# Optimization experiments

Measured on AMD Instinct MI355X. Metric: run time of the kernel, lower is better.

The kernel has to match this reference:

```python
import jax, jax.numpy as jnp
import numpy as np
from jax.scipy.linalg import solve_triangular

EPS = 1e-5
CHUNK = 64

def _rms(x, w, eps=EPS):
    return x * jax.lax.rsqrt(jnp.mean(x * x, axis=-1, keepdims=True) + eps) * w

def _l2norm(x, eps=1e-6):
    return x * jax.lax.rsqrt(jnp.sum(x * x, axis=-1, keepdims=True) + eps)

def _causal_conv(x, w):
    # x: [B,T,C], w: [C,K] depthwise causal short conv
    K = w.shape[1]
    T = x.shape[1]
    xp = jnp.pad(x, ((0, 0), (K - 1, 0), (0, 0)))
    return sum(xp[:, j:j + T, :] * w[:, j] for j in range(K))

def _chunk_gated_delta_rule(q, k, v, g, beta, chunk=CHUNK):
    # q,k: [B,H,T,Dk] (l2-normalized, q pre-scaled); v: [B,H,T,Dv]; g,beta: [B,H,T]
    Bb, H, T, Dk = k.shape
    Dv = v.shape[-1]
    N = T // chunk
    qc, kc, vc = (a.reshape(Bb, H, N, chunk, -1) for a in (q, k, v))
    gc = g.reshape(Bb, H, N, chunk)
    bc = beta.reshape(Bb, H, N, chunk)
    gcs = jnp.cumsum(gc, axis=-1)  # within-chunk cumulative log-decay
    tri = jnp.tril(jnp.ones((chunk, chunk), bool))
    tri_s = jnp.tril(jnp.ones((chunk, chunk), bool), -1)
    diff = gcs[..., :, None] - gcs[..., None, :]
    decay = jnp.where(tri, jnp.exp(jnp.where(tri, diff, 0.0)), 0.0)  # [B,H,N,C,C]
    k_beta = kc * bc[..., None]
    v_beta = vc * bc[..., None]
    A = jnp.einsum('bhnck,bhndk->bhncd', k_beta, kc) * decay
    A = jnp.where(tri_s, A, 0.0)
    eye = jnp.eye(chunk, dtype=q.dtype)
    Tmat = solve_triangular(eye + A, jnp.broadcast_to(eye, A.shape), lower=True)  # (I+A)^-1
    u = Tmat @ v_beta                               # [B,H,N,C,Dv]
    w = Tmat @ (k_beta * jnp.exp(gcs)[..., None])   # [B,H,N,C,Dk]

    def step(S, inp):
        q_i, k_i, u_i, w_i, g_i, dm_i = inp
        attn = jnp.where(tri, jnp.einsum('bhck,bhdk->bhcd', q_i, k_i) * dm_i, 0.0)
        v_new = u_i - w_i @ S
        o_i = (q_i * jnp.exp(g_i)[..., None]) @ S + attn @ v_new
        g_last = g_i[..., -1]
        k_dec = k_i * jnp.exp(g_last[..., None] - g_i)[..., None]
        S = S * jnp.exp(g_last)[..., None, None] + jnp.einsum('bhck,bhcv->bhkv', k_dec, v_new)
        return S, o_i

    xs = tuple(jnp.moveaxis(a, 2, 0) for a in (qc, kc, u, w, gcs, decay))
    S0 = jnp.zeros((Bb, H, Dk, Dv), q.dtype)
    _, outs = jax.lax.scan(step, S0, xs)  # [N,B,H,C,Dv]
    return jnp.moveaxis(outs, 0, 2).reshape(Bb, H, T, Dv)

def _layer_forward(x, mask, ln1_w, qkvz_w, ba_w, conv_w, A_log, dt_bias,
                   o_norm_w, out_w, ln2_w, gate_w, up_w, down_w):
    B, T, D = x.shape
    H = A_log.shape[0]
    kd = qkvz_w.shape[0] // 4  # key_dim == value_dim here (k_heads==v_heads, Dk==Dv)
    vd = kd
    Dk = kd // H
    Dv = vd // H
    silu = jax.nn.silu
    h = _rms(x, ln1_w)
    qkvz = h @ qkvz_w.T
    q, k, v, z = jnp.split(qkvz, [kd, 2 * kd, 2 * kd + vd], axis=-1)
    b, a = jnp.split(h @ ba_w.T, 2, axis=-1)  # [B,T,H] each
    mixed = jnp.concatenate([q, k, v], axis=-1) * mask[..., None]
    mixed = silu(_causal_conv(mixed, conv_w))
    q, k, v = jnp.split(mixed, [kd, 2 * kd], axis=-1)
    q = _l2norm(q.reshape(B, T, H, Dk))
    k = _l2norm(k.reshape(B, T, H, Dk))
    v = v.reshape(B, T, H, Dv)
    beta = jax.nn.sigmoid(b) * mask[..., None]
    g = -jnp.exp(A_log) * jax.nn.softplus(a + dt_bias) * mask[..., None]
    scale = Dk ** -0.5
    bhtd = lambda t: jnp.transpose(t, (0, 2, 1, 3))
    o = _chunk_gated_delta_rule(bhtd(q) * scale, bhtd(k), bhtd(v),
                                jnp.transpose(g, (0, 2, 1)), jnp.transpose(beta, (0, 2, 1)))
    o = jnp.transpose(o, (0, 2, 1, 3))  # [B,T,H,Dv]
    o = _rms(o, o_norm_w) * silu(z.reshape(B, T, H, Dv))  # gated RMSNorm
    x = x + o.reshape(B, T, vd) @ out_w.T
    h2 = _rms(x, ln2_w)
    mlp_out = (silu(h2 @ gate_w.T) * (h2 @ up_w.T)) @ down_w.T
    return x + mlp_out

def setup_inputs():
    key = jax.random.key(0)
    ks = jax.random.split(key, 12)
    B, T, D, H, Dk, Dv, M, K = 1, 4096, 2048, 16, 128, 128, 8192, 4
    kd, vd = H * Dk, H * Dv
    nrm = lambda i, shp, sc=0.02: jax.random.normal(ks[i], shp, jnp.float32) * sc
    return {
        'x': nrm(0, (B, T, D), 1.0),
        'mask': jnp.ones((B, T), jnp.float32),
        'ln1_w': jnp.ones((D,), jnp.float32),
        'qkvz_w': nrm(1, (2 * kd + 2 * vd, D)),
        'ba_w': nrm(2, (2 * H, D)),
        'conv_w': nrm(3, (2 * kd + vd, K), 0.3),
        'A_log': jnp.log(jax.random.uniform(ks[4], (H,), jnp.float32, 1.0, 16.0)),
        'dt_bias': nrm(5, (H,), 0.5),
        'o_norm_w': jnp.ones((Dv,), jnp.float32),
        'out_w': nrm(6, (D, vd)),
        'ln2_w': jnp.ones((D,), jnp.float32),
        'gate_w': nrm(7, (M, D)),
        'up_w': nrm(8, (M, D)),
        'down_w': nrm(9, (D, M)),
    }

def reference(x, mask, ln1_w, qkvz_w, ba_w, conv_w, A_log, dt_bias,
              o_norm_w, out_w, ln2_w, gate_w, up_w, down_w):
    return _layer_forward(x, mask, ln1_w, qkvz_w, ba_w, conv_w, A_log, dt_bias,
                          o_norm_w, out_w, ln2_w, gate_w, up_w, down_w)
```

## Files before the change

kernel.cpp:

```cpp
#include <hip/hip_runtime.h>
#include <math.h>

#define T_LEN 4096
#define DMODEL 2048
#define NH 16
#define CQKV 6144
#define CQKVZ 8192
#define SCALE 0.08838834764831845f

using bf16x8 = __attribute__((ext_vector_type(8))) short;
using f32x4  = __attribute__((ext_vector_type(4))) float;

__device__ __forceinline__ float siluf(float x) { return x / (1.0f + __expf(-x)); }

__device__ __forceinline__ unsigned short f2bf(float f) {
  unsigned int u = __float_as_uint(f);
  u = (u + 0x7FFFu + ((u >> 16) & 1u)) >> 16;
  return (unsigned short)u;
}
__device__ __forceinline__ float bf2f(unsigned short u) {
  return __uint_as_float(((unsigned int)u) << 16);
}
__device__ __forceinline__ ushort4 pack4(float a, float b, float c, float d) {
  ushort4 r; r.x = f2bf(a); r.y = f2bf(b); r.z = f2bf(c); r.w = f2bf(d); return r;
}

__device__ __forceinline__ void gl_lds16(const unsigned short* g, unsigned short* l) {
  __builtin_amdgcn_global_load_lds(
      (const __attribute__((address_space(1))) void*)g,
      (__attribute__((address_space(3))) void*)l, 16, 0, 0);
}

template<int MODE>
__global__ __launch_bounds__(256) void rmsnorm_kernel(const float* __restrict__ x,
                                                      const float* __restrict__ w,
                                                      float* __restrict__ outf,
                                                      unsigned short* __restrict__ outb) {
  const int t = blockIdx.x;
  const int tid = threadIdx.x;
  const float4* xr = (const float4*)(x + (size_t)t * DMODEL);
  float4 v0 = xr[tid];
  float4 v1 = xr[tid + 256];
  float s = v0.x*v0.x + v0.y*v0.y + v0.z*v0.z + v0.w*v0.w
          + v1.x*v1.x + v1.y*v1.y + v1.z*v1.z + v1.w*v1.w;
#pragma unroll
  for (int off = 32; off > 0; off >>= 1) s += __shfl_down(s, off);
  __shared__ float red[4];
  if ((tid & 63) == 0) red[tid >> 6] = s;
  __syncthreads();
  const float tot = red[0] + red[1] + red[2] + red[3];
  const float r = rsqrtf(tot * (1.0f / DMODEL) + 1e-5f);
  const float4* wr = (const float4*)w;
  const float4 w0 = wr[tid], w1 = wr[tid + 256];
  float4 o0, o1;
  o0.x = v0.x*r*w0.x; o0.y = v0.y*r*w0.y; o0.z = v0.z*r*w0.z; o0.w = v0.w*r*w0.w;
  o1.x = v1.x*r*w1.x; o1.y = v1.y*r*w1.y; o1.z = v1.z*r*w1.z; o1.w = v1.w*r*w1.w;
  if (MODE == 1) {
    float4* orow = (float4*)(outf + (size_t)t * DMODEL);
    orow[tid] = o0;
    orow[tid + 256] = o1;
  }
  ushort4* brow = (ushort4*)(outb + (size_t)t * DMODEL);
  brow[tid] = pack4(o0.x, o0.y, o0.z, o0.w);
  brow[tid + 256] = pack4(o1.x, o1.y, o1.z, o1.w);
}

__global__ __launch_bounds__(256) void f2b_kernel(const float* __restrict__ in,
                                                  unsigned short* __restrict__ out) {
  const size_t i = (size_t)blockIdx.x * 256 + threadIdx.x;
  const float4 a = ((const float4*)in)[2 * i];
  const float4 b = ((const float4*)in)[2 * i + 1];
  ((ushort4*)out)[2 * i] = pack4(a.x, a.y, a.z, a.w);
  ((ushort4*)out)[2 * i + 1] = pack4(b.x, b.y, b.z, b.w);
}

template<int EPI, int BM>
__global__ __launch_bounds__(512, 1) void gemm256_kernel(const unsigned short* __restrict__ A,
                                                         const unsigned short* __restrict__ B,
                                                         float* __restrict__ Cf,
                                                         unsigned short* __restrict__ Cb,
                                                         int M, int N, int K) {
  constexpr int BN = 256;
  constexpr int MI = BM / 32;
  constexpr int AW = BM / 128;
  __shared__ __align__(16) unsigned short lds[3][(BM + BN) * 32];
  const int nbm = M / BM, nbn = N / BN, nwg = nbm * nbn;
  const int nt = K >> 5;
  int bmi, bni;
  {
    const int bid = blockIdx.x;
    const int cpx = nwg >> 3;
    int sc = 1;
    while (sc * sc < cpx) sc <<= 1;
    if (sc * sc > cpx) sc >>= 1;
    const int scn = (sc > 0) ? (cpx / sc) : 0;
    if ((nwg & 7) == 0 && sc > 0 && sc * scn == cpx && (nbm % sc) == 0 && (nbn % scn) == 0) {
      const int chunk = bid & 7, widx = bid >> 3;
      const int regc = nbn / scn;
      bmi = (chunk / regc) * sc + widx / scn;
      bni = (chunk % regc) * scn + widx % scn;
    } else {
      bmi = bid / nbn; bni = bid % nbn;
    }
  }
  const int bm = bmi * BM, bn = bni * BN;
  const int tid = threadIdx.x;
  const int wv = tid >> 6, ln = tid & 63;
  const int fr = ln & 15, qq = ln >> 4;
  const int wm = wv >> 2, wn = wv & 3;
  const int ra0 = wm * (BM / 2), rb0 = wn * 64;
  const int lrow = ln >> 2;
  const int lslot = ln & 3;

  f32x4 acc[MI][4];
  const f32x4 zero = {0.f, 0.f, 0.f, 0.f};
#pragma unroll
  for (int mi = 0; mi < MI; mi++)
#pragma unroll
    for (int ni = 0; ni < 4; ni++) acc[mi][ni] = zero;

  auto stageA = [&](int buf, int t) {
    const int k0 = t << 5;
#pragma unroll
    for (int q = 0; q < AW; q++) {
      const int lr = q * 128 + wv * 16 + lrow;
      const int sl = lslot ^ ((lr >> 1) & 3);
      gl_lds16(A + (size_t)(bm + lr) * K + k0 + sl * 8,
               &lds[buf][(q * 128 + wv * 16) * 32]);
    }
  };
  auto stageB = [&](int buf, int t) {
    const int k0 = t << 5;
#pragma unroll
    for (int q = 0; q < 2; q++) {
      const int lr = q * 128 + wv * 16 + lrow;
      const int sl = lslot ^ ((lr >> 1) & 3);
      gl_lds16(B + (size_t)(bn + lr) * K + k0 + sl * 8,
               &lds[buf][BM * 32 + (q * 128 + wv * 16) * 32]);
    }
  };

  stageA(0, 0); stageB(0, 0);
  stageA(1, 1); stageB(1, 1);
  if constexpr (AW == 2) asm volatile("s_waitcnt vmcnt(4)" ::: "memory");
  else                   asm volatile("s_waitcnt vmcnt(3)" ::: "memory");
  __builtin_amdgcn_s_barrier();
  asm volatile("" ::: "memory");

  for (int t = 0; t < nt; t++) {
    const int cb = t % 3;
    const int b2 = (t + 2) % 3;
    const unsigned short* lA = &lds[cb][0];
    const unsigned short* lB = &lds[cb][BM * 32];
    bf16x8 bfr[4];
#pragma unroll
    for (int ni = 0; ni < 4; ni++) {
      const int r = rb0 + ni * 16 + fr;
      bfr[ni] = *(const bf16x8*)&lB[r * 32 + ((qq ^ ((r >> 1) & 3)) << 3)];
    }
    bf16x8 afr[MI];
#pragma unroll
    for (int mi = 0; mi < MI; mi++) {
      const int r = ra0 + mi * 16 + fr;
      afr[mi] = *(const bf16x8*)&lA[r * 32 + ((qq ^ ((r >> 1) & 3)) << 3)];
    }
    if (t + 2 < nt) { stageA(b2, t + 2); stageB(b2, t + 2); }
    __builtin_amdgcn_s_setprio(1);
#pragma unroll
    for (int mi = 0; mi < MI; mi++)
#pragma unroll
      for (int ni = 0; ni < 4; ni++)
        acc[mi][ni] = __builtin_amdgcn_mfma_f32_16x16x32_bf16(afr[mi], bfr[ni], acc[mi][ni], 0, 0, 0);
    __builtin_amdgcn_s_setprio(0);
    if (t + 1 < nt) {
      asm volatile("s_waitcnt lgkmcnt(0)" ::: "memory");
      if (t + 2 < nt) {
        if constexpr (AW == 2) asm volatile("s_waitcnt vmcnt(4)" ::: "memory");
        else                   asm volatile("s_waitcnt vmcnt(3)" ::: "memory");
      } else {
        asm volatile("s_waitcnt vmcnt(0)" ::: "memory");
      }
      __builtin_amdgcn_s_barrier();
      asm volatile("" ::: "memory");
    }
  }

  const int cm4 = qq * 4;
#pragma unroll
  for (int mi = 0; mi < MI; mi++) {
#pragma unroll
    for (int ni = 0; ni < 4; ni++) {
#pragma unroll
      for (int r = 0; r < 4; r++) {
        const int grow = bm + ra0 + mi * 16 + cm4 + r;
        const int gcol = bn + rb0 + ni * 16 + fr;
        const size_t off = (size_t)grow * N + gcol;
        const float v = acc[mi][ni][r];
        if (EPI == 0) {
          Cb[off] = f2bf(v);
        } else if (EPI == 1) {
          Cf[off] += v;
        } else {
          Cb[off] = f2bf(siluf(bf2f(Cb[off])) * v);
        }
      }
    }
  }
}

__global__ __launch_bounds__(256) void ba_gemm_kernel(const float* __restrict__ h_in,
                                                      const float* __restrict__ ba_w,
                                                      float* __restrict__ ba_out) {
  __shared__ __align__(16) float hl[2048];
  __shared__ float red[32][9];
  const int t = blockIdx.x;
  const int tid = threadIdx.x;
  const float4* hr = (const float4*)(h_in + (size_t)t * DMODEL);
  ((float4*)hl)[tid] = hr[tid];
  ((float4*)hl)[tid + 256] = hr[tid + 256];
  __syncthreads();
  const int c = tid & 31;
  const int p = tid >> 5;
  const float* wrow = ba_w + (size_t)c * DMODEL + p * 256;
  const float* hrow = hl + p * 256;
  float s = 0.f;
#pragma unroll 8
  for (int k = 0; k < 256; k++) s += hrow[k] * wrow[k];
  red[c][p] = s;
  __syncthreads();
  if (tid < 32) {
    float tot = 0.f;
#pragma unroll
    for (int q = 0; q < 8; q++) tot += red[tid][q];
    ba_out[(size_t)t * 32 + tid] = tot;
  }
}

__global__ __launch_bounds__(256) void zcopy_kernel(const unsigned short* __restrict__ qkvz,
                                                    unsigned short* __restrict__ z) {
  const int idx = blockIdx.x * 256 + threadIdx.x;
  const int t = idx >> 8;
  const int c8 = (idx & 255) * 8;
  *(uint4*)(z + (size_t)t * 2048 + c8) =
      *(const uint4*)(qkvz + (size_t)t * CQKVZ + CQKV + c8);
}

__global__ __launch_bounds__(256) void conv_silu_kernel(const unsigned short* __restrict__ qkvz,
                                                        const float* __restrict__ conv_w,
                                                        const float* __restrict__ mask,
                                                        float* __restrict__ mixed) {
  const int idx = blockIdx.x * 256 + threadIdx.x;
  const int c4 = (idx % 1536) * 4;
  const int t = idx / 1536;
  const float4 w0 = *(const float4*)(conv_w + (size_t)c4 * 4);
  const float4 w1 = *(const float4*)(conv_w + (size_t)c4 * 4 + 4);
  const float4 w2 = *(const float4*)(conv_w + (size_t)c4 * 4 + 8);
  const float4 w3 = *(const float4*)(conv_w + (size_t)c4 * 4 + 12);
  const float wj0[4] = {w0.x, w0.y, w0.z, w0.w};
  const float wj1[4] = {w1.x, w1.y, w1.z, w1.w};
  const float wj2[4] = {w2.x, w2.y, w2.z, w2.w};
  const float wj3[4] = {w3.x, w3.y, w3.z, w3.w};
  float4 acc = make_float4(0.f, 0.f, 0.f, 0.f);
#pragma unroll
  for (int j = 0; j < 4; j++) {
    const int tt = t - 3 + j;
    if (tt < 0) continue;
    const float m = mask[tt];
    const ushort4 xb = *(const ushort4*)(qkvz + (size_t)tt * CQKVZ + c4);
    acc.x += bf2f(xb.x) * m * wj0[j];
    acc.y += bf2f(xb.y) * m * wj1[j];
    acc.z += bf2f(xb.z) * m * wj2[j];
    acc.w += bf2f(xb.w) * m * wj3[j];
  }
  acc.x = siluf(acc.x); acc.y = siluf(acc.y); acc.z = siluf(acc.z); acc.w = siluf(acc.w);
  *(float4*)(mixed + (size_t)t * CQKV + c4) = acc;
}

__global__ __launch_bounds__(256) void l2norm_kernel(float* __restrict__ mixed) {
  const int r = blockIdx.x * 4 + (threadIdx.x >> 6);
  const int lane = threadIdx.x & 63;
  const int t = r >> 5;
  const int hh = r & 31;
  float* p = mixed + (size_t)t * CQKV + hh * 128 + lane * 2;
  float2 v = *(float2*)p;
  float s = v.x * v.x + v.y * v.y;
#pragma unroll
  for (int off = 32; off > 0; off >>= 1) s += __shfl_down(s, off);
  s = __shfl(s, 0);
  const float rn = rsqrtf(s + 1e-6f);
  v.x *= rn; v.y *= rn;
  *(float2*)p = v;
}

__global__ __launch_bounds__(256) void beta_g_kernel(const float* __restrict__ ba,
                                                     const float* __restrict__ A_log,
                                                     const float* __restrict__ dt_bias,
                                                     const float* __restrict__ mask,
                                                     float* __restrict__ beta,
                                                     float* __restrict__ g) {
  const int idx = blockIdx.x * 256 + threadIdx.x;
  const int t = idx >> 4;
  const int h = idx & 15;
  const float b = ba[(size_t)t * 32 + h];
  const float a = ba[(size_t)t * 32 + 16 + h];
  const float m = mask[t];
  beta[idx] = m / (1.0f + expf(-b));
  const float xx = a + dt_bias[h];
  const float sp = (xx > 20.0f) ? xx : log1pf(expf(xx));
  g[idx] = -expf(A_log[h]) * sp * m;
}

__global__ __launch_bounds__(256) void gcs_kernel(const float* __restrict__ g,
                                                  float* __restrict__ gcsbuf,
                                                  float* __restrict__ edkbuf,
                                                  float* __restrict__ egqbuf,
                                                  float* __restrict__ adecbuf) {
  const int idx = blockIdx.x * 256 + threadIdx.x;
  if (idx >= 1024) return;
  const int h = idx >> 6;
  const int n = idx & 63;
  const int t0 = n * 64;
  float s = 0.f;
  for (int i = 0; i < 64; i++) {
    s += g[(size_t)(t0 + i) * NH + h];
    gcsbuf[(size_t)idx * 64 + i] = s;
  }
  const float glast = s;
  adecbuf[idx] = __expf(glast);
  for (int i = 0; i < 64; i++) {
    const float gi = gcsbuf[(size_t)idx * 64 + i];
    edkbuf[(size_t)idx * 64 + i] = __expf(glast - gi);
    egqbuf[(size_t)idx * 64 + i] = __expf(gi) * SCALE;
  }
}

__global__ __launch_bounds__(256) void pre_attn_kernel(const float* __restrict__ mixed,
                                                       const float* __restrict__ gcsbuf,
                                                       const float* __restrict__ betabuf,
                                                       float* __restrict__ abuf,
                                                       float* __restrict__ attnbuf) {
  __shared__ __align__(16) float kl[64][132];
  __shared__ float gcs_s[64];
  __shared__ float betal[64];
  const int blk = blockIdx.x;
  const int h = blk >> 6;
  const int n = blk & 63;
  const int t0 = n * 64;
  const int tid = threadIdx.x;
  if (tid < 64) {
    gcs_s[tid] = gcsbuf[(size_t)blk * 64 + tid];
    betal[tid] = betabuf[(size_t)(t0 + tid) * NH + h];
  }
#pragma unroll
  for (int rep = 0; rep < 8; rep++) {
    const int lin = rep * 256 + tid;
    const int i = lin >> 5;
    const int d = (lin & 31) * 4;
    const float4 kv = *(const float4*)(mixed + (size_t)(t0 + i) * CQKV + 2048 + h * 128 + d);
    *(float4*)&kl[i][d] = kv;
  }
  __syncthreads();
  const int cj = tid & 15;
  const int ri = tid >> 4;
  const int i0 = ri * 4, j0 = cj * 4;
  float accA[4][4], accQ[4][4];
#pragma unroll
  for (int a = 0; a < 4; a++)
#pragma unroll
    for (int b = 0; b < 4; b++) { accA[a][b] = 0.f; accQ[a][b] = 0.f; }
  const float* qbase = mixed + (size_t)t0 * CQKV + h * 128;
#pragma unroll 4
  for (int d = 0; d < 128; d++) {
    const float kj0 = kl[j0][d], kj1 = kl[j0 + 1][d], kj2 = kl[j0 + 2][d], kj3 = kl[j0 + 3][d];
#pragma unroll
    for (int a = 0; a < 4; a++) {
      const float ka = kl[i0 + a][d];
      const float qa = qbase[(size_t)(i0 + a) * CQKV + d];
      accA[a][0] += ka * kj0; accA[a][1] += ka * kj1; accA[a][2] += ka * kj2; accA[a][3] += ka * kj3;
      accQ[a][0] += qa * kj0; accQ[a][1] += qa * kj1; accQ[a][2] += qa * kj2; accQ[a][3] += qa * kj3;
    }
  }
#pragma unroll
  for (int a = 0; a < 4; a++) {
    const int i = i0 + a;
    const float gi = gcs_s[i];
    const float bi = betal[i];
    float4 Av, Qv;
    float dec;
    dec = __expf(fminf(gi - gcs_s[j0 + 0], 0.f));
    Av.x = (i > j0 + 0) ? accA[a][0] * bi * dec : 0.f;
    Qv.x = (i >= j0 + 0) ? accQ[a][0] * dec * SCALE : 0.f;
    dec = __expf(fminf(gi - gcs_s[j0 + 1], 0.f));
    Av.y = (i > j0 + 1) ? accA[a][1] * bi * dec : 0.f;
    Qv.y = (i >= j0 + 1) ? accQ[a][1] * dec * SCALE : 0.f;
    dec = __expf(fminf(gi - gcs_s[j0 + 2], 0.f));
    Av.z = (i > j0 + 2) ? accA[a][2] * bi * dec : 0.f;
    Qv.z = (i >= j0 + 2) ? accQ[a][2] * dec * SCALE : 0.f;
    dec = __expf(fminf(gi - gcs_s[j0 + 3], 0.f));
    Av.w = (i > j0 + 3) ? accA[a][3] * bi * dec : 0.f;
    Qv.w = (i >= j0 + 3) ? accQ[a][3] * dec * SCALE : 0.f;
    *(float4*)(abuf + (size_t)blk * 4096 + i * 64 + j0) = Av;
    *(float4*)(attnbuf + (size_t)blk * 4096 + i * 64 + j0) = Qv;
  }
}

__global__ __launch_bounds__(256) void pre_solve_kernel(const float* __restrict__ abuf,
                                                        const float* __restrict__ betabuf,
                                                        float* __restrict__ tbuf) {
  __shared__ float Al[64][65];
  __shared__ float Tl[64][65];
  const int blk = blockIdx.x;
  const int h = blk >> 6;
  const int n = blk & 63;
  const int t0 = n * 64;
  const int tid = threadIdx.x;
#pragma unroll
  for (int rep = 0; rep < 4; rep++) {
    const int lin = rep * 256 + tid;
    const int i = lin >> 4;
    const int j = (lin & 15) * 4;
    const float4 av = *(const float4*)(abuf + (size_t)blk * 4096 + i * 64 + j);
    Al[i][j] = av.x; Al[i][j + 1] = av.y; Al[i][j + 2] = av.z; Al[i][j + 3] = av.w;
  }
  __syncthreads();
  if (tid < 64) {
    const int j = tid;
    const float bj = betabuf[(size_t)(t0 + j) * NH + h];
    for (int i = 0; i < 64; i++) {
      float s = (i == j) ? 1.0f : 0.0f;
      for (int l = j; l < i; l++) s -= Al[i][l] * Tl[l][j];
      Tl[i][j] = s;
    }
    for (int i = j; i < 64; i++) Tl[i][j] *= bj;
  }
  __syncthreads();
#pragma unroll
  for (int rep = 0; rep < 4; rep++) {
    const int lin = rep * 256 + tid;
    const int i = lin >> 4;
    const int j = (lin & 15) * 4;
    float4 tv;
    tv.x = Tl[i][j]; tv.y = Tl[i][j + 1]; tv.z = Tl[i][j + 2]; tv.w = Tl[i][j + 3];
    *(float4*)(tbuf + (size_t)blk * 4096 + i * 64 + j) = tv;
  }
}

__global__ __launch_bounds__(256) void pre_uw_kernel(const float* __restrict__ mixed,
                                                     const float* __restrict__ tbuf,
                                                     const float* __restrict__ gcsbuf,
                                                     float* __restrict__ ubuf,
                                                     unsigned short* __restrict__ wbf) {
  __shared__ __align__(16) float Tl[64][68];
  __shared__ __align__(16) float xl[64][132];
  __shared__ float egcs[64];
  const int blk = blockIdx.x;
  const int h = blk >> 6;
  const int n = blk & 63;
  const int t0 = n * 64;
  const int tid = threadIdx.x;
  if (tid < 64) egcs[tid] = __expf(gcsbuf[(size_t)blk * 64 + tid]);
#pragma unroll
  for (int rep = 0; rep < 4; rep++) {
    const int lin = rep * 256 + tid;
    const int i = lin >> 4;
    const int j = (lin & 15) * 4;
    const float4 tv = *(const float4*)(tbuf + (size_t)blk * 4096 + i * 64 + j);
    *(float4*)&Tl[i][j] = tv;
  }
#pragma unroll
  for (int rep = 0; rep < 8; rep++) {
    const int lin = rep * 256 + tid;
    const int i = lin >> 5;
    const int d = (lin & 31) * 4;
    const float4 vv = *(const float4*)(mixed + (size_t)(t0 + i) * CQKV + 4096 + h * 128 + d);
    *(float4*)&xl[i][d] = vv;
  }
  __syncthreads();
  const int cgu = tid & 15;
  const int riu = tid >> 4;
  const int i0 = riu * 4;
  const int d0 = cgu * 8;
  float acc[4][8];
#pragma unroll
  for (int a = 0; a < 4; a++)
#pragma unroll
    for (int b = 0; b < 8; b++) acc[a][b] = 0.f;
#pragma unroll 2
  for (int j = 0; j < 64; j++) {
    const float tv[4] = {Tl[i0][j], Tl[i0 + 1][j], Tl[i0 + 2][j], Tl[i0 + 3][j]};
    const float4 x0 = *(const float4*)&xl[j][d0];
    const float4 x1 = *(const float4*)&xl[j][d0 + 4];
    const float xv[8] = {x0.x, x0.y, x0.z, x0.w, x1.x, x1.y, x1.z, x1.w};
#pragma unroll
    for (int a = 0; a < 4; a++)
#pragma unroll
      for (int b = 0; b < 8; b++) acc[a][b] += tv[a] * xv[b];
  }
#pragma unroll
  for (int a = 0; a < 4; a++) {
    float* up = ubuf + (size_t)(t0 + i0 + a) * 2048 + h * 128 + d0;
    *(float4*)up = make_float4(acc[a][0], acc[a][1], acc[a][2], acc[a][3]);
    *(float4*)(up + 4) = make_float4(acc[a][4], acc[a][5], acc[a][6], acc[a][7]);
  }
  __syncthreads();
#pragma unroll
  for (int rep = 0; rep < 8; rep++) {
    const int lin = rep * 256 + tid;
    const int i = lin >> 5;
    const int d = (lin & 31) * 4;
    float4 kv = *(const float4*)(mixed + (size_t)(t0 + i) * CQKV + 2048 + h * 128 + d);
    const float e = egcs[i];
    kv.x *= e; kv.y *= e; kv.z *= e; kv.w *= e;
    *(float4*)&xl[i][d] = kv;
  }
  __syncthreads();
#pragma unroll
  for (int a = 0; a < 4; a++)
#pragma unroll
    for (int b = 0; b < 8; b++) acc[a][b] = 0.f;
#pragma unroll 2
  for (int j = 0; j < 64; j++) {
    const float tv[4] = {Tl[i0][j], Tl[i0 + 1][j], Tl[i0 + 2][j], Tl[i0 + 3][j]};
    const float4 x0 = *(const float4*)&xl[j][d0];
    const float4 x1 = *(const float4*)&xl[j][d0 + 4];
    const float xv[8] = {x0.x, x0.y, x0.z, x0.w, x1.x, x1.y, x1.z, x1.w};
#pragma unroll
    for (int a = 0; a < 4; a++)
#pragma unroll
      for (int b = 0; b < 8; b++) acc[a][b] += tv[a] * xv[b];
  }
#pragma unroll
  for (int a = 0; a < 4; a++) {
    unsigned short* wp = wbf + (size_t)(t0 + i0 + a) * 2048 + h * 128 + d0;
    *(ushort4*)wp = pack4(acc[a][0], acc[a][1], acc[a][2], acc[a][3]);
    *(ushort4*)(wp + 4) = pack4(acc[a][4], acc[a][5], acc[a][6], acc[a][7]);
  }
}

__global__ __launch_bounds__(256) void ktrans_kernel(const float* __restrict__ mixed,
                                                     const float* __restrict__ edkbuf,
                                                     const float* __restrict__ egqbuf,
                                                     unsigned short* __restrict__ kdT,
                                                     unsigned short* __restrict__ qe) {
  __shared__ __align__(16) float kl[64][132];
  __shared__ float edk_s[64];
  __shared__ float egq_s[64];
  const int blk = blockIdx.x;
  const int h = blk >> 6;
  const int n = blk & 63;
  const int t0 = n * 64;
  const int tid = threadIdx.x;
  if (tid < 64) {
    edk_s[tid] = edkbuf[(size_t)blk * 64 + tid];
    egq_s[tid] = egqbuf[(size_t)blk * 64 + tid];
  }
#pragma unroll
  for (int q = 0; q < 8; q++) {
    const int idx = tid + q * 256;
    const int l = idx >> 5, c4 = (idx & 31) * 4;
    *(float4*)&kl[l][c4] = *(const float4*)(mixed + (size_t)(t0 + l) * CQKV + 2048 + h * 128 + c4);
  }
  __syncthreads();
#pragma unroll
  for (int q = 0; q < 4; q++) {
    const int idx = tid + q * 256;
    const int d = idx >> 3, l8 = (idx & 7) * 8;
    float v[8];
#pragma unroll
    for (int j = 0; j < 8; j++) v[j] = kl[l8 + j][d] * edk_s[l8 + j];
    unsigned short* p = kdT + (size_t)blk * 8192 + d * 64 + l8;
    *(ushort4*)p = pack4(v[0], v[1], v[2], v[3]);
    *(ushort4*)(p + 4) = pack4(v[4], v[5], v[6], v[7]);
  }
#pragma unroll
  for (int q = 0; q < 8; q++) {
    const int idx = tid + q * 256;
    const int i = idx >> 5, c4 = (idx & 31) * 4;
    const float4 v = *(const float4*)(mixed + (size_t)(t0 + i) * CQKV + h * 128 + c4);
    const float e = egq_s[i];
    *(ushort4*)(qe + (size_t)(t0 + i) * 2048 + h * 128 + c4) =
        pack4(v.x * e, v.y * e, v.z * e, v.w * e);
  }
}

__global__ __launch_bounds__(512) void scan_kernel(const unsigned short* __restrict__ wbf,
                                                   const unsigned short* __restrict__ kdT,
                                                   const float* __restrict__ ubuf,
                                                   const float* __restrict__ adecbuf,
                                                   unsigned short* __restrict__ STb,
                                                   unsigned short* __restrict__ vtb,
                                                   const float* __restrict__ gw,
                                                   const float* __restrict__ uw,
                                                   const float* __restrict__ dw,
                                                   const float* __restrict__ ow,
                                                   const float* __restrict__ xin,
                                                   unsigned short* __restrict__ Wg,
                                                   unsigned short* __restrict__ Wu,
                                                   unsigned short* __restrict__ Wd,
                                                   unsigned short* __restrict__ Wo,
                                                   float* __restrict__ outc) {
  __shared__ __align__(16) unsigned short w_lds[64 * 128];
  __shared__ __align__(16) unsigned short kT_lds[128 * 64];
  __shared__ __align__(16) unsigned short st_lds[128 * 128];
  __shared__ __align__(16) unsigned short vt_lds[128 * 64];
  __shared__ __align__(16) float u_lds[64 * 132];
  if (blockIdx.x >= 16) {
    const int xb = blockIdx.x - 16;
    const int tid = threadIdx.x;
    if (xb < 13312) {
      const float* src;
      unsigned short* dst;
      size_t u;
      if (xb < 4096)       { src = gw; dst = Wg; u = (size_t)xb * 512 + tid; }
      else if (xb < 8192)  { src = uw; dst = Wu; u = (size_t)(xb - 4096) * 512 + tid; }
      else if (xb < 12288) { src = dw; dst = Wd; u = (size_t)(xb - 8192) * 512 + tid; }
      else                 { src = ow; dst = Wo; u = (size_t)(xb - 12288) * 512 + tid; }
      const float4 a = ((const float4*)src)[2 * u];
      const float4 b = ((const float4*)src)[2 * u + 1];
      ((ushort4*)dst)[2 * u] = pack4(a.x, a.y, a.z, a.w);
      ((ushort4*)dst)[2 * u + 1] = pack4(b.x, b.y, b.z, b.w);
    } else {
      const size_t i = (size_t)(xb - 13312) * 512 + tid;
      ((float4*)outc)[i] = ((const float4*)xin)[i];
    }
    return;
  }
  const int h = blockIdx.x;
  const int tid = threadIdx.x;
  const int ln = tid & 63;
  const int wv = tid >> 6;
  const int fr = ln & 15;
  const int g = ln >> 4;
  const int lt = wv & 3;
  const int ch = wv >> 2;
  const f32x4 zero = {0.f, 0.f, 0.f, 0.f};

  uint4 wreg[2], kreg[2];
  float4 ureg[4];
#pragma unroll
  for (int q = 0; q < 2; q++) {
    const int idx = tid + q * 512;
    const int row = idx >> 4, c8 = (idx & 15) * 8;
    wreg[q] = *(const uint4*)(wbf + (size_t)row * 2048 + h * 128 + c8);
    const int d = idx >> 3, l8 = (idx & 7) * 8;
    kreg[q] = *(const uint4*)(kdT + (size_t)(h * 64) * 8192 + d * 64 + l8);
  }
#pragma unroll
  for (int q = 0; q < 4; q++) {
    const int idx = tid + q * 512;
    const int row = idx >> 5, c4 = (idx & 31) * 4;
    ureg[q] = *(const float4*)(ubuf + (size_t)row * 2048 + h * 128 + c4);
  }

  f32x4 acc2[8];
#pragma unroll
  for (int ct = 0; ct < 8; ct++) acc2[ct] = zero;

  for (int n = 0; n < 64; n++) {
    const int blk = h * 64 + n;
#pragma unroll
    for (int q = 0; q < 2; q++) {
      const int idx = tid + q * 512;
      const int row = idx >> 4, c8 = (idx & 15) * 8;
      *(uint4*)&w_lds[row * 128 + (((c8 >> 3) ^ (row & 7)) << 3)] = wreg[q];
    }
#pragma unroll
    for (int q = 0; q < 4; q++) {
      const int idx = tid + q * 512;
      const int row = idx >> 5, c4 = (idx & 31) * 4;
      *(float4*)&u_lds[row * 132 + c4] = ureg[q];
    }
    {
      const int db = wv * 16 + g * 4;
#pragma unroll
      for (int ct = 0; ct < 8; ct++) {
        const int c = ct * 16 + fr;
        *(ushort4*)&st_lds[c * 128 + (((db >> 3) ^ (c & 7)) << 3) + (db & 7)] =
            pack4(acc2[ct][0], acc2[ct][1], acc2[ct][2], acc2[ct][3]);
      }
    }
    asm volatile("s_waitcnt lgkmcnt(0)" ::: "memory");
    __builtin_amdgcn_sched_barrier(0);
    asm volatile("s_barrier" ::: "memory");
    __builtin_amdgcn_sched_barrier(0);
#pragma unroll
    for (int q = 0; q < 2; q++) {
      const int idx = tid + q * 512;
      const int d = idx >> 3, l8 = (idx & 7) * 8;
      *(uint4*)&kT_lds[d * 64 + (((l8 >> 3) ^ (d & 7)) << 3)] = kreg[q];
    }
    if (n < 63) {
      const int t0n = (n + 1) * 64;
#pragma unroll
      for (int q = 0; q < 2; q++) {
        const int idx = tid + q * 512;
        const int row = idx >> 4, c8 = (idx & 15) * 8;
        wreg[q] = *(const uint4*)(wbf + (size_t)(t0n + row) * 2048 + h * 128 + c8);
        const int d = idx >> 3, l8 = (idx & 7) * 8;
        kreg[q] = *(const uint4*)(kdT + (size_t)(blk + 1) * 8192 + d * 64 + l8);
      }
#pragma unroll
      for (int q = 0; q < 4; q++) {
        const int idx = tid + q * 512;
        const int row = idx >> 5, c4 = (idx & 31) * 4;
        ureg[q] = *(const float4*)(ubuf + (size_t)(t0n + row) * 2048 + h * 128 + c4);
      }
    }
#pragma unroll
    for (int q = 0; q < 4; q++) {
      const int idx = tid + q * 512;
      const int c = idx >> 4, dg = idx & 15;
      *(uint4*)(STb + (size_t)blk * 16384 + c * 128 + dg * 8) =
          *(const uint4*)&st_lds[c * 128 + ((dg ^ (c & 7)) << 3)];
    }
    f32x4 acc1[4];
#pragma unroll
    for (int ct = 0; ct < 4; ct++) acc1[ct] = zero;
#pragma unroll
    for (int ks = 0; ks < 4; ks++) {
      const int kb = ks * 4 + g;
      const int ar = lt * 16 + fr;
      const bf16x8 a = *(const bf16x8*)&w_lds[ar * 128 + ((kb ^ (ar & 7)) << 3)];
#pragma unroll
      for (int ct = 0; ct < 4; ct++) {
        const int c = (ch * 4 + ct) * 16 + fr;
        const bf16x8 b = *(const bf16x8*)&st_lds[c * 128 + ((kb ^ (c & 7)) << 3)];
        acc1[ct] = __builtin_amdgcn_mfma_f32_16x16x32_bf16(a, b, acc1[ct], 0, 0, 0);
      }
    }
    {
      const int lb = lt * 16 + g * 4;
#pragma unroll
      for (int ct = 0; ct < 4; ct++) {
        const int c = (ch * 4 + ct) * 16 + fr;
        const float v0 = u_lds[(lb + 0) * 132 + c] - acc1[ct][0];
        const float v1 = u_lds[(lb + 1) * 132 + c] - acc1[ct][1];
        const float v2 = u_lds[(lb + 2) * 132 + c] - acc1[ct][2];
        const float v3 = u_lds[(lb + 3) * 132 + c] - acc1[ct][3];
        *(ushort4*)&vt_lds[c * 64 + (((lb >> 3) ^ (c & 7)) << 3) + (lb & 7)] =
            pack4(v0, v1, v2, v3);
      }
    }
    const float adec = adecbuf[blk];
    asm volatile("s_waitcnt lgkmcnt(0)" ::: "memory");
    __builtin_amdgcn_sched_barrier(0);
    asm volatile("s_barrier" ::: "memory");
    __builtin_amdgcn_sched_barrier(0);
#pragma unroll
    for (int q = 0; q < 2; q++) {
      const int idx = tid + q * 512;
      const int c = idx >> 3, lg = idx & 7;
      *(uint4*)(vtb + (size_t)blk * 8192 + c * 64 + lg * 8) =
          *(const uint4*)&vt_lds[c * 64 + ((lg ^ (c & 7)) << 3)];
    }
#pragma unroll
    for (int ct = 0; ct < 8; ct++) {
      acc2[ct][0] *= adec; acc2[ct][1] *= adec; acc2[ct][2] *= adec; acc2[ct][3] *= adec;
    }
#pragma unroll
    for (int ks = 0; ks < 2; ks++) {
      const int kb = ks * 4 + g;
      const int ar = wv * 16 + fr;
      const bf16x8 a = *(const bf16x8*)&kT_lds[ar * 64 + ((kb ^ (ar & 7)) << 3)];
#pragma unroll
      for (int ct = 0; ct < 8; ct++) {
        const int c = ct * 16 + fr;
        const bf16x8 b = *(const bf16x8*)&vt_lds[c * 64 + ((kb ^ (c & 7)) << 3)];
        acc2[ct] = __builtin_amdgcn_mfma_f32_16x16x32_bf16(a, b, acc2[ct], 0, 0, 0);
      }
    }
  }
}

__global__ __launch_bounds__(256) void ocomp_kernel(const unsigned short* __restrict__ qe,
                                                    const unsigned short* __restrict__ STbuf,
                                                    const unsigned short* __restrict__ vtbuf,
                                                    const float* __restrict__ attnbuf,
                                                    const unsigned short* __restrict__ zb,
                                                    const float* __restrict__ onw,
                                                    unsigned short* __restrict__ ob) {
  __shared__ __align__(16) unsigned short STl[128 * 128];
  __shared__ __align__(16) unsigned short vtl[128 * 64];
  __shared__ __align__(16) unsigned short ql[64 * 128];
  __shared__ __align__(16) unsigned short al[64 * 64];
  const int blk = blockIdx.x;
  const int h = blk >> 6;
  const int n = blk & 63;
  const int t0 = n * 64;
  const int tid = threadIdx.x;
#pragma unroll
  for (int q = 0; q < 8; q++) {
    const int idx = tid + q * 256;
    const int c = idx >> 4, dg = idx & 15;
    *(uint4*)&STl[c * 128 + ((dg ^ (c & 7)) << 3)] =
        *(const uint4*)(STbuf + (size_t)blk * 16384 + c * 128 + dg * 8);
  }
#pragma unroll
  for (int q = 0; q < 4; q++) {
    const int idx = tid + q * 256;
    const int c = idx >> 3, lg = idx & 7;
    *(uint4*)&vtl[c * 64 + ((lg ^ (c & 7)) << 3)] =
        *(const uint4*)(vtbuf + (size_t)blk * 8192 + c * 64 + lg * 8);
  }
#pragma unroll
  for (int q = 0; q < 4; q++) {
    const int idx = tid + q * 256;
    const int i = idx >> 4, dg = idx & 15;
    *(uint4*)&ql[i * 128 + ((dg ^ (i & 7)) << 3)] =
        *(const uint4*)(qe + (size_t)(t0 + i) * 2048 + h * 128 + dg * 8);
  }
#pragma unroll
  for (int q = 0; q < 4; q++) {
    const int idx = tid + q * 256;
    const int i = idx >> 4, l4 = (idx & 15) * 4;
    const float4 v = *(const float4*)(attnbuf + (size_t)blk * 4096 + i * 64 + l4);
    *(ushort4*)&al[i * 64 + (((l4 >> 3) ^ (i & 7)) << 3) + (l4 & 7)] =
        pack4(v.x, v.y, v.z, v.w);
  }
  __syncthreads();
  const int ln = tid & 63;
  const int wv = tid >> 6;
  const int fr = ln & 15;
  const int g = ln >> 4;
  const int i0 = wv * 16;
  f32x4 acc[8];
  const f32x4 zero = {0.f, 0.f, 0.f, 0.f};
#pragma unroll
  for (int nt = 0; nt < 8; nt++) acc[nt] = zero;
#pragma unroll
  for (int ks = 0; ks < 4; ks++) {
    const int kb = ks * 4 + g;
    const int ar = i0 + fr;
    const bf16x8 a = *(const bf16x8*)&ql[ar * 128 + ((kb ^ (ar & 7)) << 3)];
#pragma unroll
    for (int nt = 0; nt < 8; nt++) {
      const int c = nt * 16 + fr;
      const bf16x8 b = *(const bf16x8*)&STl[c * 128 + ((kb ^ (c & 7)) << 3)];
      acc[nt] = __builtin_amdgcn_mfma_f32_16x16x32_bf16(a, b, acc[nt], 0, 0, 0);
    }
  }
#pragma unroll
  for (int ks = 0; ks < 2; ks++) {
    const int kb = ks * 4 + g;
    const int ar = i0 + fr;
    const bf16x8 a = *(const bf16x8*)&al[ar * 64 + ((kb ^ (ar & 7)) << 3)];
#pragma unroll
    for (int nt = 0; nt < 8; nt++) {
      const int c = nt * 16 + fr;
      const bf16x8 b = *(const bf16x8*)&vtl[c * 64 + ((kb ^ (c & 7)) << 3)];
      acc[nt] = __builtin_amdgcn_mfma_f32_16x16x32_bf16(a, b, acc[nt], 0, 0, 0);
    }
  }
  float s0 = 0.f, s1 = 0.f, s2 = 0.f, s3 = 0.f;
#pragma unroll
  for (int nt = 0; nt < 8; nt++) {
    s0 += acc[nt][0] * acc[nt][0];
    s1 += acc[nt][1] * acc[nt][1];
    s2 += acc[nt][2] * acc[nt][2];
    s3 += acc[nt][3] * acc[nt][3];
  }
#pragma unroll
  for (int m = 1; m < 16; m <<= 1) {
    s0 += __shfl_xor(s0, m);
    s1 += __shfl_xor(s1, m);
    s2 += __shfl_xor(s2, m);
    s3 += __shfl_xor(s3, m);
  }
  float rn[4];
  rn[0] = rsqrtf(s0 * (1.0f / 128.0f) + 1e-5f);
  rn[1] = rsqrtf(s1 * (1.0f / 128.0f) + 1e-5f);
  rn[2] = rsqrtf(s2 * (1.0f / 128.0f) + 1e-5f);
  rn[3] = rsqrtf(s3 * (1.0f / 128.0f) + 1e-5f);
#pragma unroll
  for (int nt = 0; nt < 8; nt++) {
    const int c = nt * 16 + fr;
    const float wn = onw[c];
#pragma unroll
    for (int r = 0; r < 4; r++) {
      const size_t off = (size_t)(t0 + i0 + g * 4 + r) * 2048 + h * 128 + c;
      const float zz = siluf(bf2f(zb[off]));
      ob[off] = f2bf(acc[nt][r] * rn[r] * wn * zz);
    }
  }
}

extern "C" void kernel_launch(void* const* d_in, const int* in_sizes, int n_in,
                              void* d_out, int out_size, void* d_ws, size_t ws_size,
                              hipStream_t stream) {
  (void)in_sizes; (void)n_in; (void)out_size;
  const float* x        = (const float*)d_in[0];
  const float* mask     = (const float*)d_in[1];
  const float* ln1_w    = (const float*)d_in[2];
  const float* qkvz_w   = (const float*)d_in[3];
  const float* ba_w     = (const float*)d_in[4];
  const float* conv_w   = (const float*)d_in[5];
  const float* A_log    = (const float*)d_in[6];
  const float* dt_bias  = (const float*)d_in[7];
  const float* o_norm_w = (const float*)d_in[8];
  const float* out_w    = (const float*)d_in[9];
  const float* ln2_w    = (const float*)d_in[10];
  const float* gate_w   = (const float*)d_in[11];
  const float* up_w     = (const float*)d_in[12];
  const float* down_w   = (const float*)d_in[13];
  float* out = (float*)d_out;

  const size_t NEED_BYTES = (size_t)75825152 * 4;
  if (ws_size < NEED_BYTES) return;

  float* ws = (float*)d_ws;
  float* mixed_buf = ws;
  unsigned short* Wg = (unsigned short*)ws;
  unsigned short* Wu = (unsigned short*)(ws + 8388608);
  unsigned short* Wd = (unsigned short*)(ws + 16777216);
  unsigned short* qkvz_bf = (unsigned short*)(ws + 25165824);
  float* u_buf = ws + 25165824;
  unsigned short* wbf = (unsigned short*)(ws + 33554432);
  unsigned short* kdT = (unsigned short*)(ws + 37748736);
  unsigned short* gate_bf = (unsigned short*)(ws + 25165824);
  unsigned short* z_bf = (unsigned short*)(ws + 41943040);
  float* h_buf = ws + 46137344;
  float* a_buf = ws + 46137344;
  unsigned short* vt_buf = (unsigned short*)(ws + 46137344);
  float* t_buf = ws + 50331648;
  unsigned short* qe_bf = (unsigned short*)(ws + 50331648);
  unsigned short* h_bf  = (unsigned short*)(ws + 54525952);
  unsigned short* ob    = (unsigned short*)(ws + 54525952);
  unsigned short* h2_bf = (unsigned short*)(ws + 54525952);
  float* attn_buf = ws + 58720256;
  unsigned short* Wq = (unsigned short*)(ws + 62914560);
  unsigned short* ST_buf = (unsigned short*)(ws + 62914560);
  unsigned short* Wo = (unsigned short*)(ws + 71303168);
  float* ba_buf   = ws + 73400320;
  float* beta_buf = ws + 73531392;
  float* g_buf    = ws + 73596928;
  float* gcs_buf  = ws + 73662464;
  float* edk_buf  = ws + 73728000;
  float* egq_buf  = ws + 73793536;
  float* adec_buf = ws + 73859072;

  rmsnorm_kernel<1><<<4096, 256, 0, stream>>>(x, ln1_w, h_buf, h_bf);
  f2b_kernel<<<8192, 256, 0, stream>>>(qkvz_w, Wq);
  gemm256_kernel<0, 256><<<512, 512, 0, stream>>>(h_bf, Wq, nullptr, qkvz_bf, 4096, 8192, 2048);
  ba_gemm_kernel<<<4096, 256, 0, stream>>>(h_buf, ba_w, ba_buf);
  zcopy_kernel<<<4096, 256, 0, stream>>>(qkvz_bf, z_bf);
  conv_silu_kernel<<<24576, 256, 0, stream>>>(qkvz_bf, conv_w, mask, mixed_buf);
  l2norm_kernel<<<32768, 256, 0, stream>>>(mixed_buf);
  beta_g_kernel<<<256, 256, 0, stream>>>(ba_buf, A_log, dt_bias, mask, beta_buf, g_buf);
  gcs_kernel<<<4, 256, 0, stream>>>(g_buf, gcs_buf, edk_buf, egq_buf, adec_buf);
  pre_attn_kernel<<<1024, 256, 0, stream>>>(mixed_buf, gcs_buf, beta_buf, a_buf, attn_buf);
  pre_solve_kernel<<<1024, 256, 0, stream>>>(a_buf, beta_buf, t_buf);
  pre_uw_kernel<<<1024, 256, 0, stream>>>(mixed_buf, t_buf, gcs_buf, u_buf, wbf);
  ktrans_kernel<<<1024, 256, 0, stream>>>(mixed_buf, edk_buf, egq_buf, kdT, qe_bf);
  scan_kernel<<<17424, 512, 0, stream>>>(wbf, kdT, u_buf, adec_buf, ST_buf, vt_buf,
                                         gate_w, up_w, down_w, out_w, x,
                                         Wg, Wu, Wd, Wo, out);
  ocomp_kernel<<<1024, 256, 0, stream>>>(qe_bf, ST_buf, vt_buf, attn_buf,
                                         z_bf, o_norm_w, ob);
  gemm256_kernel<1, 128><<<256, 512, 0, stream>>>(ob, Wo, out, nullptr, 4096, 2048, 2048);
  rmsnorm_kernel<2><<<4096, 256, 0, stream>>>(out, ln2_w, nullptr, h2_bf);
  gemm256_kernel<0, 256><<<512, 512, 0, stream>>>(h2_bf, Wg, nullptr, gate_bf, 4096, 8192, 2048);
  gemm256_kernel<2, 256><<<512, 512, 0, stream>>>(h2_bf, Wu, nullptr, gate_bf, 4096, 8192, 2048);
  gemm256_kernel<1, 128><<<256, 512, 0, stream>>>(gate_bf, Wd, out, nullptr, 4096, 2048, 8192);
}
```

Before: 1.481 ms.

## Restructure scan kernel with per-wave private state, async LDS staging and pre-swizzled inputs

```diff
diff --git a/kernel.cpp b/kernel.cpp
--- a/kernel.cpp
+++ b/kernel.cpp
@@ -531,9 +531,10 @@
   }
 #pragma unroll
   for (int a = 0; a < 4; a++) {
-    unsigned short* wp = wbf + (size_t)(t0 + i0 + a) * 2048 + h * 128 + d0;
-    *(ushort4*)wp = pack4(acc[a][0], acc[a][1], acc[a][2], acc[a][3]);
-    *(ushort4*)(wp + 4) = pack4(acc[a][4], acc[a][5], acc[a][6], acc[a][7]);
+    const int l = i0 + a;
+    unsigned short* wp = wbf + (size_t)(t0 + l) * 2048 + h * 128 + ((cgu ^ (l & 7)) << 3);
+    *(ushort4*)wp = pack4(-acc[a][0], -acc[a][1], -acc[a][2], -acc[a][3]);
+    *(ushort4*)(wp + 4) = pack4(-acc[a][4], -acc[a][5], -acc[a][6], -acc[a][7]);
   }
 }
 
@@ -564,11 +565,12 @@
 #pragma unroll
   for (int q = 0; q < 4; q++) {
     const int idx = tid + q * 256;
-    const int d = idx >> 3, l8 = (idx & 7) * 8;
+    const int d = idx >> 3, lsl = idx & 7;
+    const int l8 = lsl * 8;
     float v[8];
 #pragma unroll
     for (int j = 0; j < 8; j++) v[j] = kl[l8 + j][d] * edk_s[l8 + j];
-    unsigned short* p = kdT + (size_t)blk * 8192 + d * 64 + l8;
+    unsigned short* p = kdT + (size_t)blk * 8192 + d * 64 + ((lsl ^ (d & 7)) << 3);
     *(ushort4*)p = pack4(v[0], v[1], v[2], v[3]);
     *(ushort4*)(p + 4) = pack4(v[4], v[5], v[6], v[7]);
   }
@@ -583,45 +585,41 @@
   }
 }
 
-__global__ __launch_bounds__(512) void scan_kernel(const unsigned short* __restrict__ wbf,
-                                                   const unsigned short* __restrict__ kdT,
-                                                   const float* __restrict__ ubuf,
-                                                   const float* __restrict__ adecbuf,
-                                                   unsigned short* __restrict__ STb,
-                                                   unsigned short* __restrict__ vtb,
-                                                   const float* __restrict__ gw,
-                                                   const float* __restrict__ uw,
-                                                   const float* __restrict__ dw,
-                                                   const float* __restrict__ ow,
-                                                   const float* __restrict__ xin,
-                                                   unsigned short* __restrict__ Wg,
-                                                   unsigned short* __restrict__ Wu,
-                                                   unsigned short* __restrict__ Wd,
-                                                   unsigned short* __restrict__ Wo,
-                                                   float* __restrict__ outc) {
-  __shared__ __align__(16) unsigned short w_lds[64 * 128];
-  __shared__ __align__(16) unsigned short kT_lds[128 * 64];
-  __shared__ __align__(16) unsigned short st_lds[128 * 128];
-  __shared__ __align__(16) unsigned short vt_lds[128 * 64];
-  __shared__ __align__(16) float u_lds[64 * 132];
+__global__ __launch_bounds__(256, 1) void scan_kernel(const unsigned short* __restrict__ wbf,
+                                                      const unsigned short* __restrict__ kdT,
+                                                      const float* __restrict__ ubuf,
+                                                      const float* __restrict__ adecbuf,
+                                                      unsigned short* __restrict__ STb,
+                                                      unsigned short* __restrict__ vtb,
+                                                      const float* __restrict__ gw,
+                                                      const float* __restrict__ uw,
+                                                      const float* __restrict__ dw,
+                                                      const float* __restrict__ ow,
+                                                      const float* __restrict__ xin,
+                                                      unsigned short* __restrict__ Wg,
+                                                      unsigned short* __restrict__ Wu,
+                                                      unsigned short* __restrict__ Wd,
+                                                      unsigned short* __restrict__ Wo,
+                                                      float* __restrict__ outc) {
+  __shared__ __align__(16) unsigned short stage[2][16384];
+  __shared__ __align__(16) unsigned short privAll[4][6144];
   if (blockIdx.x >= 16) {
     const int xb = blockIdx.x - 16;
     const int tid = threadIdx.x;
-    if (xb < 13312) {
-      const float* src;
-      unsigned short* dst;
-      size_t u;
-      if (xb < 4096)       { src = gw; dst = Wg; u = (size_t)xb * 512 + tid; }
-      else if (xb < 8192)  { src = uw; dst = Wu; u = (size_t)(xb - 4096) * 512 + tid; }
-      else if (xb < 12288) { src = dw; dst = Wd; u = (size_t)(xb - 8192) * 512 + tid; }
-      else                 { src = ow; dst = Wo; u = (size_t)(xb - 12288) * 512 + tid; }
+    if (xb < 26624) {
+      const float* src; unsigned short* dst; size_t u;
+      if (xb < 8192)       { src = gw; dst = Wg; u = (size_t)xb * 256 + tid; }
+      else if (xb < 16384) { src = uw; dst = Wu; u = (size_t)(xb - 8192) * 256 + tid; }
+      else if (xb < 24576) { src = dw; dst = Wd; u = (size_t)(xb - 16384) * 256 + tid; }
+      else                 { src = ow; dst = Wo; u = (size_t)(xb - 24576) * 256 + tid; }
       const float4 a = ((const float4*)src)[2 * u];
       const float4 b = ((const float4*)src)[2 * u + 1];
       ((ushort4*)dst)[2 * u] = pack4(a.x, a.y, a.z, a.w);
       ((ushort4*)dst)[2 * u + 1] = pack4(b.x, b.y, b.z, b.w);
     } else {
-      const size_t i = (size_t)(xb - 13312) * 512 + tid;
-      ((float4*)outc)[i] = ((const float4*)xin)[i];
+      const size_t i = (size_t)(xb - 26624) * 256 + tid;
+      ((float4*)outc)[2 * i] = ((const float4*)xin)[2 * i];
+      ((float4*)outc)[2 * i + 1] = ((const float4*)xin)[2 * i + 1];
     }
     return;
   }
@@ -630,144 +628,128 @@
   const int ln = tid & 63;
   const int wv = tid >> 6;
   const int fr = ln & 15;
-  const int g = ln >> 4;
-  const int lt = wv & 3;
-  const int ch = wv >> 2;
+  const int g  = ln >> 4;
+  const int c0 = wv * 32;
+  const int fsw = fr & 7;
+  unsigned short* privA = &privAll[wv][0];
+  unsigned short* privB = &privAll[wv][4096];
   const f32x4 zero = {0.f, 0.f, 0.f, 0.f};
 
-  uint4 wreg[2], kreg[2];
-  float4 ureg[4];
-#pragma unroll
-  for (int q = 0; q < 2; q++) {
-    const int idx = tid + q * 512;
-    const int row = idx >> 4, c8 = (idx & 15) * 8;
-    wreg[q] = *(const uint4*)(wbf + (size_t)row * 2048 + h * 128 + c8);
-    const int d = idx >> 3, l8 = (idx & 7) * 8;
-    kreg[q] = *(const uint4*)(kdT + (size_t)(h * 64) * 8192 + d * 64 + l8);
-  }
-#pragma unroll
-  for (int q = 0; q < 4; q++) {
-    const int idx = tid + q * 512;
-    const int row = idx >> 5, c4 = (idx & 31) * 4;
-    ureg[q] = *(const float4*)(ubuf + (size_t)row * 2048 + h * 128 + c4);
-  }
-
-  f32x4 acc2[8];
-#pragma unroll
-  for (int ct = 0; ct < 8; ct++) acc2[ct] = zero;
+  f32x4 acc2[8][2];
+#pragma unroll
+  for (int dt = 0; dt < 8; dt++)
+#pragma unroll
+    for (int ct = 0; ct < 2; ct++) acc2[dt][ct] = zero;
+
+  auto stage_wk = [&](int buf, int n1) {
+    const int t0n = n1 * 64;
+    const size_t kbase = (size_t)(h * 64 + n1) * 8192;
+#pragma unroll
+    for (int q = 0; q < 4; q++) {
+      const int rw = (wv * 4 + q) * 4 + (ln >> 4);
+      gl_lds16(wbf + (size_t)(t0n + rw) * 2048 + h * 128 + (ln & 15) * 8,
+               &stage[buf][(wv * 4 + q) * 512]);
+      const int rk = (wv * 4 + q) * 8 + (ln >> 3);
+      gl_lds16(kdT + kbase + rk * 64 + (ln & 7) * 8,
+               &stage[buf][8192 + (wv * 4 + q) * 512]);
+    }
+  };
+
+  stage_wk(0, 0);
+  asm volatile("s_waitcnt vmcnt(0)" ::: "memory");
+  __builtin_amdgcn_s_barrier();
+  asm volatile("" ::: "memory");
 
   for (int n = 0; n < 64; n++) {
     const int blk = h * 64 + n;
-#pragma unroll
-    for (int q = 0; q < 2; q++) {
-      const int idx = tid + q * 512;
-      const int row = idx >> 4, c8 = (idx & 15) * 8;
-      *(uint4*)&w_lds[row * 128 + (((c8 >> 3) ^ (row & 7)) << 3)] = wreg[q];
-    }
-#pragma unroll
-    for (int q = 0; q < 4; q++) {
-      const int idx = tid + q * 512;
-      const int row = idx >> 5, c4 = (idx & 31) * 4;
-      *(float4*)&u_lds[row * 132 + c4] = ureg[q];
-    }
-    {
-      const int db = wv * 16 + g * 4;
-#pragma unroll
-      for (int ct = 0; ct < 8; ct++) {
+    const int t0 = n * 64;
+    const unsigned short* wl = &stage[n & 1][0];
+    const unsigned short* kl = &stage[n & 1][8192];
+    float ur[4][2][4];
+#pragma unroll
+    for (int lt = 0; lt < 4; lt++)
+#pragma unroll
+      for (int ct = 0; ct < 2; ct++)
+#pragma unroll
+        for (int r = 0; r < 4; r++)
+          ur[lt][ct][r] = ubuf[(size_t)(t0 + lt * 16 + g * 4 + r) * 2048 + h * 128 + c0 + ct * 16 + fr];
+    const float adec = adecbuf[blk];
+    __builtin_amdgcn_sched_barrier(0);
+    if (n + 1 < 64) stage_wk((n + 1) & 1, n + 1);
+    __builtin_amdgcn_sched_barrier(0);
+#pragma unroll
+    for (int dt = 0; dt < 8; dt++)
+#pragma unroll
+      for (int ct = 0; ct < 2; ct++) {
         const int c = ct * 16 + fr;
-        *(ushort4*)&st_lds[c * 128 + (((db >> 3) ^ (c & 7)) << 3) + (db & 7)] =
-            pack4(acc2[ct][0], acc2[ct][1], acc2[ct][2], acc2[ct][3]);
+        const int slot = dt * 2 + (g >> 1);
+        const ushort4 pv = pack4(acc2[dt][ct][0], acc2[dt][ct][1], acc2[dt][ct][2], acc2[dt][ct][3]);
+        *(ushort4*)&privA[c * 128 + ((slot ^ fsw) << 3) + (g & 1) * 4] = pv;
+        *(ushort4*)(STb + (size_t)blk * 16384 + (c0 + c) * 128 + dt * 16 + g * 4) = pv;
       }
-    }
-    asm volatile("s_waitcnt lgkmcnt(0)" ::: "memory");
-    __builtin_amdgcn_sched_barrier(0);
-    asm volatile("s_barrier" ::: "memory");
-    __builtin_amdgcn_sched_barrier(0);
-#pragma unroll
-    for (int q = 0; q < 2; q++) {
-      const int idx = tid + q * 512;
-      const int d = idx >> 3, l8 = (idx & 7) * 8;
-      *(uint4*)&kT_lds[d * 64 + (((l8 >> 3) ^ (d & 7)) << 3)] = kreg[q];
-    }
-    if (n < 63) {
-      const int t0n = (n + 1) * 64;
-#pragma unroll
-      for (int q = 0; q < 2; q++) {
-        const int idx = tid + q * 512;
-        const int row = idx >> 4, c8 = (idx & 15) * 8;
-        wreg[q] = *(const uint4*)(wbf + (size_t)(t0n + row) * 2048 + h * 128 + c8);
-        const int d = idx >> 3, l8 = (idx & 7) * 8;
-        kreg[q] = *(const uint4*)(kdT + (size_t)(blk + 1) * 8192 + d * 64 + l8);
+    f32x4 acc1[4][2];
+#pragma unroll
+    for (int lt = 0; lt < 4; lt++)
+#pragma unroll
+      for (int ct = 0; ct < 2; ct++) {
+        f32x4 t;
+        t[0] = ur[lt][ct][0]; t[1] = ur[lt][ct][1]; t[2] = ur[lt][ct][2]; t[3] = ur[lt][ct][3];
+        acc1[lt][ct] = t;
       }
-#pragma unroll
-      for (int q = 0; q < 4; q++) {
-        const int idx = tid + q * 512;
-        const int row = idx >> 5, c4 = (idx & 31) * 4;
-        ureg[q] = *(const float4*)(ubuf + (size_t)(t0n + row) * 2048 + h * 128 + c4);
-      }
-    }
-#pragma unroll
-    for (int q = 0; q < 4; q++) {
-      const int idx = tid + q * 512;
-      const int c = idx >> 4, dg = idx & 15;
-      *(uint4*)(STb + (size_t)blk * 16384 + c * 128 + dg * 8) =
-          *(const uint4*)&st_lds[c * 128 + ((dg ^ (c & 7)) << 3)];
-    }
-    f32x4 acc1[4];
-#pragma unroll
-    for (int ct = 0; ct < 4; ct++) acc1[ct] = zero;
 #pragma unroll
     for (int ks = 0; ks < 4; ks++) {
       const int kb = ks * 4 + g;
-      const int ar = lt * 16 + fr;
-      const bf16x8 a = *(const bf16x8*)&w_lds[ar * 128 + ((kb ^ (ar & 7)) << 3)];
-#pragma unroll
-      for (int ct = 0; ct < 4; ct++) {
-        const int c = (ch * 4 + ct) * 16 + fr;
-        const bf16x8 b = *(const bf16x8*)&st_lds[c * 128 + ((kb ^ (c & 7)) << 3)];
-        acc1[ct] = __builtin_amdgcn_mfma_f32_16x16x32_bf16(a, b, acc1[ct], 0, 0, 0);
+      bf16x8 bfr[2];
+#pragma unroll
+      for (int ct = 0; ct < 2; ct++)
+        bfr[ct] = *(const bf16x8*)&privA[(ct * 16 + fr) * 128 + ((kb ^ fsw) << 3)];
+#pragma unroll
+      for (int lt = 0; lt < 4; lt++) {
+        const bf16x8 a = *(const bf16x8*)&wl[(lt * 16 + fr) * 128 + ((kb ^ fsw) << 3)];
+#pragma unroll
+        for (int ct = 0; ct < 2; ct++)
+          acc1[lt][ct] = __builtin_amdgcn_mfma_f32_16x16x32_bf16(a, bfr[ct], acc1[lt][ct], 0, 0, 0);
       }
     }
-    {
-      const int lb = lt * 16 + g * 4;
-#pragma unroll
-      for (int ct = 0; ct < 4; ct++) {
-        const int c = (ch * 4 + ct) * 16 + fr;
-        const float v0 = u_lds[(lb + 0) * 132 + c] - acc1[ct][0];
-        const float v1 = u_lds[(lb + 1) * 132 + c] - acc1[ct][1];
-        const float v2 = u_lds[(lb + 2) * 132 + c] - acc1[ct][2];
-        const float v3 = u_lds[(lb + 3) * 132 + c] - acc1[ct][3];
-        *(ushort4*)&vt_lds[c * 64 + (((lb >> 3) ^ (c & 7)) << 3) + (lb & 7)] =
-            pack4(v0, v1, v2, v3);
+#pragma unroll
+    for (int lt = 0; lt < 4; lt++)
+#pragma unroll
+      for (int ct = 0; ct < 2; ct++) {
+        const int c = ct * 16 + fr;
+        const int slot = lt * 2 + (g >> 1);
+        const ushort4 pv = pack4(acc1[lt][ct][0], acc1[lt][ct][1], acc1[lt][ct][2], acc1[lt][ct][3]);
+        *(ushort4*)&privB[c * 64 + ((slot ^ fsw) << 3) + (g & 1) * 4] = pv;
+        *(ushort4*)(vtb + (size_t)blk * 8192 + (c0 + c) * 64 + lt * 16 + g * 4) = pv;
       }
-    }
-    const float adec = adecbuf[blk];
-    asm volatile("s_waitcnt lgkmcnt(0)" ::: "memory");
-    __builtin_amdgcn_sched_barrier(0);
-    asm volatile("s_barrier" ::: "memory");
-    __builtin_amdgcn_sched_barrier(0);
-#pragma unroll
-    for (int q = 0; q < 2; q++) {
-      const int idx = tid + q * 512;
-      const int c = idx >> 3, lg = idx & 7;
-      *(uint4*)(vtb + (size_t)blk * 8192 + c * 64 + lg * 8) =
-          *(const uint4*)&vt_lds[c * 64 + ((lg ^ (c & 7)) << 3)];
-    }
-#pragma unroll
-    for (int ct = 0; ct < 8; ct++) {
-      acc2[ct][0] *= adec; acc2[ct][1] *= adec; acc2[ct][2] *= adec; acc2[ct][3] *= adec;
-    }
+#pragma unroll
+    for (int dt = 0; dt < 8; dt++)
+#pragma unroll
+      for (int ct = 0; ct < 2; ct++) {
+        acc2[dt][ct][0] *= adec; acc2[dt][ct][1] *= adec;
+        acc2[dt][ct][2] *= adec; acc2[dt][ct][3] *= adec;
+      }
 #pragma unroll
     for (int ks = 0; ks < 2; ks++) {
       const int kb = ks * 4 + g;
-      const int ar = wv * 16 + fr;
-      const bf16x8 a = *(const bf16x8*)&kT_lds[ar * 64 + ((kb ^ (ar & 7)) << 3)];
-#pragma unroll
-      for (int ct = 0; ct < 8; ct++) {
-        const int c = ct * 16 + fr;
-        const bf16x8 b = *(const bf16x8*)&vt_lds[c * 64 + ((kb ^ (c & 7)) << 3)];
-        acc2[ct] = __builtin_amdgcn_mfma_f32_16x16x32_bf16(a, b, acc2[ct], 0, 0, 0);
+      bf16x8 bfr[2];
+#pragma unroll
+      for (int ct = 0; ct < 2; ct++)
+        bfr[ct] = *(const bf16x8*)&privB[(ct * 16 + fr) * 64 + ((kb ^ fsw) << 3)];
+#pragma unroll
+      for (int dt = 0; dt < 8; dt++) {
+        const bf16x8 a = *(const bf16x8*)&kl[(dt * 16 + fr) * 64 + ((kb ^ fsw) << 3)];
+#pragma unroll
+        for (int ct = 0; ct < 2; ct++)
+          acc2[dt][ct] = __builtin_amdgcn_mfma_f32_16x16x32_bf16(a, bfr[ct], acc2[dt][ct], 0, 0, 0);
       }
+    }
+    if (n + 1 < 64) {
+      asm volatile("s_waitcnt lgkmcnt(0)" ::: "memory");
+      __builtin_amdgcn_sched_barrier(0);
+      asm volatile("s_waitcnt vmcnt(24)" ::: "memory");
+      __builtin_amdgcn_sched_barrier(0);
+      __builtin_amdgcn_s_barrier();
+      __builtin_amdgcn_sched_barrier(0);
     }
   }
 }
@@ -951,7 +933,7 @@
   pre_solve_kernel<<<1024, 256, 0, stream>>>(a_buf, beta_buf, t_buf);
   pre_uw_kernel<<<1024, 256, 0, stream>>>(mixed_buf, t_buf, gcs_buf, u_buf, wbf);
   ktrans_kernel<<<1024, 256, 0, stream>>>(mixed_buf, edk_buf, egq_buf, kdT, qe_bf);
-  scan_kernel<<<17424, 512, 0, stream>>>(wbf, kdT, u_buf, adec_buf, ST_buf, vt_buf,
+  scan_kernel<<<30736, 256, 0, stream>>>(wbf, kdT, u_buf, adec_buf, ST_buf, vt_buf,
                                          gate_w, up_w, down_w, out_w, x,
                                          Wg, Wu, Wd, Wo, out);
   ocomp_kernel<<<1024, 256, 0, stream>>>(qe_bf, ST_buf, vt_buf, attn_buf,
```

Measured after the change: 1.509 ms. No clear change (+1.9%).
